# Kernel tuning notes

Measured on AMD Instinct MI355X. Metric: run time of the kernel, lower is better.

## Reference

```python
import jax, jax.numpy as jnp
import numpy as np


def setup_inputs() -> dict:
    key0 = jax.random.key(0)
    kq, kk, kv = jax.random.split(key0, 3)
    B, S, D = 16, 2048, 64  # batch*heads, seq_len, head_dim
    return {
        "query": jax.random.normal(kq, (B, S, D), dtype=jnp.float32),
        "key": jax.random.normal(kk, (B, S, D), dtype=jnp.float32),
        "value": jax.random.normal(kv, (B, S, D), dtype=jnp.float32),
    }


def reference(query, key, value):
    # context = K @ V^T : [B, S, S]  (the seq x seq intermediate the kernel should avoid)
    context = jnp.einsum("bkd,bvd->bkv", key, value)
    # attention = context^T @ Q : [B, S, D]
    attention = jnp.einsum("bkv,bkd->bvd", context, query)
    return attention
```

## Files before the change

kernel.cpp:

```cpp
#include <hip/hip_runtime.h>


typedef float vf4 __attribute__((ext_vector_type(4)));
typedef float vf2 __attribute__((ext_vector_type(2)));

#define BATCH 16
#define SEQ   2048
#define DIM   64
#define SCHUNK 128
#define NCHUNK (SEQ / SCHUNK)
#define RBLK  64
#define TPAD  68

__global__ __launch_bounds__(512) void ktq_kernel(const float* __restrict__ K,
                                                  const float* __restrict__ Q,
                                                  float* __restrict__ M) {
    __shared__ float Ks[SCHUNK * DIM];
    __shared__ float Qs[SCHUNK * DIM];
    const int b     = blockIdx.y;
    const int chunk = blockIdx.x;
    const int t     = threadIdx.x;

    const float* Kb = K + (size_t)b * SEQ * DIM + (size_t)chunk * SCHUNK * DIM;
    const float* Qb = Q + (size_t)b * SEQ * DIM + (size_t)chunk * SCHUNK * DIM;

#pragma unroll
    for (int i = 0; i < 4; ++i) {
        int idx = i * 512 + t;
        ((vf4*)Ks)[idx] = __builtin_nontemporal_load(&((const vf4*)Kb)[idx]);
        ((vf4*)Qs)[idx] = __builtin_nontemporal_load(&((const vf4*)Qb)[idx]);
    }
    __syncthreads();

    const int tx = t & 15;
    const int ty = t >> 4;
    float acc[2][4];
#pragma unroll
    for (int i = 0; i < 2; ++i)
#pragma unroll
        for (int j = 0; j < 4; ++j) acc[i][j] = 0.f;

    for (int s = 0; s < SCHUNK; ++s) {
        vf2 ak = *(const vf2*)&Ks[s * DIM + ty * 2];
        vf4 bq = *(const vf4*)&Qs[s * DIM + tx * 4];
#pragma unroll
        for (int i = 0; i < 2; ++i)
#pragma unroll
            for (int j = 0; j < 4; ++j) acc[i][j] += ak[i] * bq[j];
    }

    float* Mb = M + b * DIM * DIM;
#pragma unroll
    for (int i = 0; i < 2; ++i)
#pragma unroll
        for (int j = 0; j < 4; ++j)
            atomicAdd(&Mb[(ty * 2 + i) * DIM + tx * 4 + j], acc[i][j]);
}

__global__ __launch_bounds__(256) void vm_kernel(const float* __restrict__ V,
                                                 const float* __restrict__ M,
                                                 float* __restrict__ O) {
    __shared__ float Ml[DIM * DIM];
    __shared__ float VsT[DIM * TPAD];
    const int b  = blockIdx.y;
    const int rb = blockIdx.x;
    const int t  = threadIdx.x;

    const float* Mb = M + b * DIM * DIM;
    const float* Vb = V + (size_t)b * SEQ * DIM + (size_t)rb * RBLK * DIM;

#pragma unroll
    for (int i = 0; i < 4; ++i) {
        int idx = i * 256 + t;
        ((vf4*)Ml)[idx] = ((const vf4*)Mb)[idx];
    }
#pragma unroll
    for (int i = 0; i < 4; ++i) {
        int idx = i * 256 + t;
        int row = idx >> 4;
        int col = (idx & 15) * 4;
        vf4 v = __builtin_nontemporal_load(&((const vf4*)Vb)[idx]);
        VsT[(col + 0) * TPAD + row] = v[0];
        VsT[(col + 1) * TPAD + row] = v[1];
        VsT[(col + 2) * TPAD + row] = v[2];
        VsT[(col + 3) * TPAD + row] = v[3];
    }
    __syncthreads();

    const int tx = t & 15;
    const int ty = t >> 4;
    float acc[4][4];
#pragma unroll
    for (int i = 0; i < 4; ++i)
#pragma unroll
        for (int j = 0; j < 4; ++j) acc[i][j] = 0.f;

    for (int dp = 0; dp < DIM; ++dp) {
        vf4 mv = *(const vf4*)&Ml[dp * DIM + tx * 4];
        vf4 av = *(const vf4*)&VsT[dp * TPAD + ty * 4];
#pragma unroll
        for (int i = 0; i < 4; ++i)
#pragma unroll
            for (int j = 0; j < 4; ++j) acc[i][j] += av[i] * mv[j];
    }

    float* Ob = O + (size_t)b * SEQ * DIM + (size_t)rb * RBLK * DIM;
#pragma unroll
    for (int i = 0; i < 4; ++i) {
        vf4 o = {acc[i][0], acc[i][1], acc[i][2], acc[i][3]};
        __builtin_nontemporal_store(o, (vf4*)&Ob[(ty * 4 + i) * DIM + tx * 4]);
    }
}

extern "C" void kernel_launch(void* const* d_in, const int* in_sizes, int n_in,
                              void* d_out, int out_size, void* d_ws, size_t ws_size,
                              hipStream_t stream) {
    const float* Q = (const float*)d_in[0];
    const float* K = (const float*)d_in[1];
    const float* V = (const float*)d_in[2];
    float* O = (float*)d_out;
    float* M = (float*)d_ws;

    (void)hipMemsetAsync(M, 0, (size_t)BATCH * DIM * DIM * sizeof(float), stream);

    dim3 gridA(NCHUNK, BATCH);
    ktq_kernel<<<gridA, 512, 0, stream>>>(K, Q, M);

    dim3 gridB(SEQ / RBLK, BATCH);
    vm_kernel<<<gridB, 256, 0, stream>>>(V, M, O);
}
```

Measured before the change: 104.5 us.

## Fuse both GEMM stages into one cooperative kernel with grid sync

```diff
diff --git a/kernel.cpp b/kernel.cpp
--- a/kernel.cpp
+++ b/kernel.cpp
@@ -1,4 +1,7 @@
 #include <hip/hip_runtime.h>
+#include <hip/hip_cooperative_groups.h>
+
+namespace cg = cooperative_groups;
 
 
 typedef float vf4 __attribute__((ext_vector_type(4)));
@@ -9,106 +12,101 @@
 #define DIM   64
 #define SCHUNK 128
 #define NCHUNK (SEQ / SCHUNK)
-#define RBLK  64
-#define TPAD  68
+#define NBLOCKS (BATCH * NCHUNK)
+#define ROWS2 128
+#define TPADR 132
 
-__global__ __launch_bounds__(512) void ktq_kernel(const float* __restrict__ K,
-                                                  const float* __restrict__ Q,
-                                                  float* __restrict__ M) {
-    __shared__ float Ks[SCHUNK * DIM];
-    __shared__ float Qs[SCHUNK * DIM];
-    const int b     = blockIdx.y;
-    const int chunk = blockIdx.x;
-    const int t     = threadIdx.x;
+__global__ __launch_bounds__(512, 2) void fused_attn_kernel(
+        const float* __restrict__ Q, const float* __restrict__ K,
+        const float* __restrict__ V, float* __restrict__ O,
+        float* __restrict__ P) {
+    __shared__ float smem[16384];
+    const int bx = blockIdx.x;
+    const int t  = threadIdx.x;
+    const int b  = bx >> 4;
+    const int cx = bx & 15;
+    const int tx = t & 15;
+    const int ty = t >> 4;
 
-    const float* Kb = K + (size_t)b * SEQ * DIM + (size_t)chunk * SCHUNK * DIM;
-    const float* Qb = Q + (size_t)b * SEQ * DIM + (size_t)chunk * SCHUNK * DIM;
+    {
+        float* Ks = smem;
+        float* Qs = smem + SCHUNK * DIM;
+        const float* Kb = K + ((size_t)b * SEQ + (size_t)cx * SCHUNK) * DIM;
+        const float* Qb = Q + ((size_t)b * SEQ + (size_t)cx * SCHUNK) * DIM;
 
 #pragma unroll
-    for (int i = 0; i < 4; ++i) {
-        int idx = i * 512 + t;
-        ((vf4*)Ks)[idx] = __builtin_nontemporal_load(&((const vf4*)Kb)[idx]);
-        ((vf4*)Qs)[idx] = __builtin_nontemporal_load(&((const vf4*)Qb)[idx]);
-    }
-    __syncthreads();
+        for (int i = 0; i < 4; ++i) {
+            int idx = i * 512 + t;
+            ((vf4*)Ks)[idx] = __builtin_nontemporal_load(&((const vf4*)Kb)[idx]);
+            ((vf4*)Qs)[idx] = __builtin_nontemporal_load(&((const vf4*)Qb)[idx]);
+        }
+        __syncthreads();
 
-    const int tx = t & 15;
-    const int ty = t >> 4;
-    float acc[2][4];
+        float acc[2][4] = {};
+        for (int s = 0; s < SCHUNK; ++s) {
+            vf2 ak = *(const vf2*)&Ks[s * DIM + ty * 2];
+            vf4 bq = *(const vf4*)&Qs[s * DIM + tx * 4];
 #pragma unroll
-    for (int i = 0; i < 2; ++i)
+            for (int i = 0; i < 2; ++i)
 #pragma unroll
-        for (int j = 0; j < 4; ++j) acc[i][j] = 0.f;
+                for (int j = 0; j < 4; ++j) acc[i][j] += ak[i] * bq[j];
+        }
 
-    for (int s = 0; s < SCHUNK; ++s) {
-        vf2 ak = *(const vf2*)&Ks[s * DIM + ty * 2];
-        vf4 bq = *(const vf4*)&Qs[s * DIM + tx * 4];
-#pragma unroll
-        for (int i = 0; i < 2; ++i)
-#pragma unroll
-            for (int j = 0; j < 4; ++j) acc[i][j] += ak[i] * bq[j];
+        float* Pb = P + (size_t)bx * DIM * DIM;
+        vf4 r0 = {acc[0][0], acc[0][1], acc[0][2], acc[0][3]};
+        vf4 r1 = {acc[1][0], acc[1][1], acc[1][2], acc[1][3]};
+        *(vf4*)&Pb[(ty * 2 + 0) * DIM + tx * 4] = r0;
+        *(vf4*)&Pb[(ty * 2 + 1) * DIM + tx * 4] = r1;
     }
 
-    float* Mb = M + b * DIM * DIM;
-#pragma unroll
-    for (int i = 0; i < 2; ++i)
-#pragma unroll
-        for (int j = 0; j < 4; ++j)
-            atomicAdd(&Mb[(ty * 2 + i) * DIM + tx * 4 + j], acc[i][j]);
-}
+    __threadfence();
+    cg::this_grid().sync();
 
-__global__ __launch_bounds__(256) void vm_kernel(const float* __restrict__ V,
-                                                 const float* __restrict__ M,
-                                                 float* __restrict__ O) {
-    __shared__ float Ml[DIM * DIM];
-    __shared__ float VsT[DIM * TPAD];
-    const int b  = blockIdx.y;
-    const int rb = blockIdx.x;
-    const int t  = threadIdx.x;
-
-    const float* Mb = M + b * DIM * DIM;
-    const float* Vb = V + (size_t)b * SEQ * DIM + (size_t)rb * RBLK * DIM;
+    {
+        float* Ml  = smem;
+        float* VsT = smem + DIM * DIM;
+        const float* Pb = P + (size_t)(b * NCHUNK) * DIM * DIM;
 
 #pragma unroll
-    for (int i = 0; i < 4; ++i) {
-        int idx = i * 256 + t;
-        ((vf4*)Ml)[idx] = ((const vf4*)Mb)[idx];
-    }
+        for (int i = 0; i < 2; ++i) {
+            int idx = i * 512 + t;
+            vf4 sum = ((const vf4*)Pb)[idx];
 #pragma unroll
-    for (int i = 0; i < 4; ++i) {
-        int idx = i * 256 + t;
-        int row = idx >> 4;
-        int col = (idx & 15) * 4;
-        vf4 v = __builtin_nontemporal_load(&((const vf4*)Vb)[idx]);
-        VsT[(col + 0) * TPAD + row] = v[0];
-        VsT[(col + 1) * TPAD + row] = v[1];
-        VsT[(col + 2) * TPAD + row] = v[2];
-        VsT[(col + 3) * TPAD + row] = v[3];
-    }
-    __syncthreads();
+            for (int c = 1; c < NCHUNK; ++c)
+                sum += ((const vf4*)(Pb + (size_t)c * DIM * DIM))[idx];
+            ((vf4*)Ml)[idx] = sum;
+        }
 
-    const int tx = t & 15;
-    const int ty = t >> 4;
-    float acc[4][4];
+        const float* Vb = V + ((size_t)b * SEQ + (size_t)cx * ROWS2) * DIM;
 #pragma unroll
-    for (int i = 0; i < 4; ++i)
+        for (int i = 0; i < 4; ++i) {
+            int idx = i * 512 + t;
+            int row = idx >> 4;
+            int col = (idx & 15) * 4;
+            vf4 v = __builtin_nontemporal_load(&((const vf4*)Vb)[idx]);
+            VsT[(col + 0) * TPADR + row] = v[0];
+            VsT[(col + 1) * TPADR + row] = v[1];
+            VsT[(col + 2) * TPADR + row] = v[2];
+            VsT[(col + 3) * TPADR + row] = v[3];
+        }
+        __syncthreads();
+
+        float acc[4][4] = {};
+        for (int dp = 0; dp < DIM; ++dp) {
+            vf4 mv = *(const vf4*)&Ml[dp * DIM + tx * 4];
+            vf4 av = *(const vf4*)&VsT[dp * TPADR + ty * 4];
 #pragma unroll
-        for (int j = 0; j < 4; ++j) acc[i][j] = 0.f;
+            for (int i = 0; i < 4; ++i)
+#pragma unroll
+                for (int j = 0; j < 4; ++j) acc[i][j] += av[i] * mv[j];
+        }
 
-    for (int dp = 0; dp < DIM; ++dp) {
-        vf4 mv = *(const vf4*)&Ml[dp * DIM + tx * 4];
-        vf4 av = *(const vf4*)&VsT[dp * TPAD + ty * 4];
+        float* Ob = O + ((size_t)b * SEQ + (size_t)cx * ROWS2) * DIM;
 #pragma unroll
-        for (int i = 0; i < 4; ++i)
-#pragma unroll
-            for (int j = 0; j < 4; ++j) acc[i][j] += av[i] * mv[j];
-    }
-
-    float* Ob = O + (size_t)b * SEQ * DIM + (size_t)rb * RBLK * DIM;
-#pragma unroll
-    for (int i = 0; i < 4; ++i) {
-        vf4 o = {acc[i][0], acc[i][1], acc[i][2], acc[i][3]};
-        __builtin_nontemporal_store(o, (vf4*)&Ob[(ty * 4 + i) * DIM + tx * 4]);
+        for (int i = 0; i < 4; ++i) {
+            vf4 o = {acc[i][0], acc[i][1], acc[i][2], acc[i][3]};
+            __builtin_nontemporal_store(o, (vf4*)&Ob[(ty * 4 + i) * DIM + tx * 4]);
+        }
     }
 }
 
@@ -119,13 +117,9 @@
     const float* K = (const float*)d_in[1];
     const float* V = (const float*)d_in[2];
     float* O = (float*)d_out;
-    float* M = (float*)d_ws;
+    float* P = (float*)d_ws;
 
-    (void)hipMemsetAsync(M, 0, (size_t)BATCH * DIM * DIM * sizeof(float), stream);
-
-    dim3 gridA(NCHUNK, BATCH);
-    ktq_kernel<<<gridA, 512, 0, stream>>>(K, Q, M);
-
-    dim3 gridB(SEQ / RBLK, BATCH);
-    vm_kernel<<<gridB, 256, 0, stream>>>(V, M, O);
+    void* args[] = {(void*)&Q, (void*)&K, (void*)&V, (void*)&O, (void*)&P};
+    (void)hipLaunchCooperativeKernel((void*)fused_attn_kernel,
+                                     dim3(NBLOCKS), dim3(512), args, 0, stream);
 }
```

Result: slower. 169.5 us (+62.1%).
